# Optimization experiments

Measured on AMD Instinct MI355X. Metric: run time of the kernel, lower is better.

The kernel has to match this reference:

```python
import jax, jax.numpy as jnp
import numpy as np

N_NODES = 50000


def _sage_mean(x, src, dst, Wl, bl, Wr, n_nodes):
    # PyG SAGEConv (aggr='mean', root_weight=True): lin_l(mean_j x_j) + lin_r(x_i)
    msgs = x[src]                                             # [E, F] gather
    agg = jax.ops.segment_sum(msgs, dst, num_segments=n_nodes)  # [N, F]
    cnt = jax.ops.segment_sum(jnp.ones((src.shape[0],), x.dtype), dst,
                              num_segments=n_nodes)           # [N]
    mean = agg / jnp.maximum(cnt, 1.0)[:, None]
    return mean @ Wl + bl + x @ Wr


def setup_inputs() -> dict:
    key = jax.random.key(0)
    ks = jax.random.split(key, 12)
    in_ft = 64
    o0, o1, o2 = 64, 128, 128
    d2 = o0 + o0          # conv2 in = 128
    d3 = o0 + o0 + o1     # conv3 in = 256
    E = 800000

    def lin(k, fi, fo):
        s = 1.0 / np.sqrt(fi)
        return jax.random.uniform(k, (fi, fo), jnp.float32, -s, s)

    x = jax.random.normal(ks[0], (N_NODES, in_ft), jnp.float32)
    edge_index = jax.random.randint(ks[1], (2, E), 0, N_NODES, jnp.int64)
    return {
        "x": x,
        "edge_index": edge_index,
        "Wp": lin(ks[2], in_ft, o0), "bp": jnp.zeros((o0,), jnp.float32),
        "Wl1": lin(ks[3], in_ft, o0), "bl1": jnp.zeros((o0,), jnp.float32),
        "Wr1": lin(ks[4], in_ft, o0),
        "Wl2": lin(ks[5], d2, o1), "bl2": jnp.zeros((o1,), jnp.float32),
        "Wr2": lin(ks[6], d2, o1),
        "Wl3": lin(ks[7], d3, o2), "bl3": jnp.zeros((o2,), jnp.float32),
        "Wr3": lin(ks[8], d3, o2),
    }


def reference(x, edge_index, Wp, bp, Wl1, bl1, Wr1, Wl2, bl2, Wr2, Wl3, bl3, Wr3):
    src, dst = edge_index[0], edge_index[1]
    act = jax.nn.relu
    x_p = act(x @ Wp + bp)                                        # [N, o0]
    h1 = act(_sage_mean(x, src, dst, Wl1, bl1, Wr1, N_NODES))      # [N, o0]
    in2 = jnp.concatenate([x_p, h1], axis=1)                      # [N, 2*o0]
    h2 = act(_sage_mean(in2, src, dst, Wl2, bl2, Wr2, N_NODES))    # [N, o1]
    in3 = jnp.concatenate([x_p, h1, h2], axis=1)                  # [N, 2*o0+o1]
    h3 = act(_sage_mean(in3, src, dst, Wl3, bl3, Wr3, N_NODES))    # [N, o2]
    return h3
```

## Files before the change

kernel.cpp:

```cpp
#include <hip/hip_runtime.h>

#define N_NODES 50000
#define ELLW 48

typedef unsigned int uint;
typedef unsigned short ushort;
typedef float floatx4 __attribute__((ext_vector_type(4)));
typedef short short8 __attribute__((ext_vector_type(8)));

__device__ inline ushort f2bf(float f) {
    uint u = __float_as_uint(f);
    return (ushort)((u + 0x7fffu + ((u >> 16) & 1u)) >> 16);
}
__device__ inline float bflo(uint u) { return __uint_as_float(u << 16); }
__device__ inline float bfhi(uint u) { return __uint_as_float(u & 0xffff0000u); }
__device__ inline uint pack2(float lo, float hi) {
    return (uint)f2bf(lo) | ((uint)f2bf(hi) << 16);
}

__device__ inline void swz_body(const float* __restrict__ W, ushort* __restrict__ Wz,
                                int O, int t) {
    int lane = t & 63, cb = t >> 6;
    int NBm = O / 16;
    int c = cb / NBm, nb = cb % NBm;
    int quad = lane >> 4, l16 = lane & 15;
#pragma unroll
    for (int j = 0; j < 8; j++) {
        float v = W[(size_t)(c * 32 + quad * 8 + j) * O + nb * 16 + l16];
        Wz[(size_t)t * 8 + j] = f2bf(v);
    }
}

__device__ void gemm1_body(int gb, const float* __restrict__ x,
                           const float* __restrict__ Wp, const float* __restrict__ bp,
                           const float* __restrict__ Wl1, const float* __restrict__ Wr1,
                           ushort* __restrict__ feats, ushort* __restrict__ g1in,
                           ushort* __restrict__ r1, ushort* ldsA) {
    constexpr int LDA = 40;
    const int tid = threadIdx.x;
    const int wave = tid >> 6, lane = tid & 63;
    const int quad = lane >> 4, l16 = lane & 15;
    const int node0 = gb * 64;

    floatx4 aP[4], aY[4], aR[4];
#pragma unroll
    for (int nb = 0; nb < 4; nb++) {
        aP[nb] = (floatx4){0, 0, 0, 0};
        aY[nb] = (floatx4){0, 0, 0, 0};
        aR[nb] = (floatx4){0, 0, 0, 0};
    }

#pragma unroll
    for (int kk = 0; kk < 2; kk++) {
        const int k0 = kk * 32;
        __syncthreads();
        {
            int row = tid >> 2, seg = tid & 3;
            int node = node0 + row;
            float4 v0 = {0, 0, 0, 0}, v1 = {0, 0, 0, 0};
            if (node < N_NODES) {
                v0 = *(const float4*)&x[(size_t)node * 64 + k0 + seg * 8];
                v1 = *(const float4*)&x[(size_t)node * 64 + k0 + seg * 8 + 4];
            }
            ushort4 o0, o1;
            o0.x = f2bf(v0.x); o0.y = f2bf(v0.y); o0.z = f2bf(v0.z); o0.w = f2bf(v0.w);
            o1.x = f2bf(v1.x); o1.y = f2bf(v1.y); o1.z = f2bf(v1.z); o1.w = f2bf(v1.w);
            *(ushort4*)&ldsA[row * LDA + seg * 8] = o0;
            *(ushort4*)&ldsA[row * LDA + seg * 8 + 4] = o1;
        }
        __syncthreads();

        short8 a = *(const short8*)&ldsA[(wave * 16 + l16) * LDA + quad * 8];
#pragma unroll
        for (int nb = 0; nb < 4; nb++) {
            short8 bw;
#pragma unroll
            for (int j = 0; j < 8; j++)
                bw[j] = (short)f2bf(Wp[(size_t)(k0 + quad * 8 + j) * 64 + nb * 16 + l16]);
            aP[nb] = __builtin_amdgcn_mfma_f32_16x16x32_bf16(a, bw, aP[nb], 0, 0, 0);
#pragma unroll
            for (int j = 0; j < 8; j++)
                bw[j] = (short)f2bf(Wl1[(size_t)(k0 + quad * 8 + j) * 64 + nb * 16 + l16]);
            aY[nb] = __builtin_amdgcn_mfma_f32_16x16x32_bf16(a, bw, aY[nb], 0, 0, 0);
#pragma unroll
            for (int j = 0; j < 8; j++)
                bw[j] = (short)f2bf(Wr1[(size_t)(k0 + quad * 8 + j) * 64 + nb * 16 + l16]);
            aR[nb] = __builtin_amdgcn_mfma_f32_16x16x32_bf16(a, bw, aR[nb], 0, 0, 0);
        }
    }

#pragma unroll
    for (int nb = 0; nb < 4; nb++) {
        int ncol = nb * 16 + l16;
        float bv = bp[ncol];
#pragma unroll
        for (int r = 0; r < 4; r++) {
            int node = node0 + wave * 16 + quad * 4 + r;
            if (node >= N_NODES) continue;
            ushort xp = f2bf(fmaxf(aP[nb][r] + bv, 0.f));
            feats[(size_t)node * 256 + ncol] = xp;
            g1in[(size_t)node * 128 + 64 + ncol] = xp;
            g1in[(size_t)node * 128 + ncol] = f2bf(aY[nb][r]);
            r1[(size_t)node * 64 + ncol] = f2bf(aR[nb][r]);
        }
    }
}

__global__ __launch_bounds__(256) void k1_mega(
    const int* __restrict__ src, const int* __restrict__ dst, int E,
    int* __restrict__ fillc, ushort* __restrict__ ell,
    const float* __restrict__ x,
    const float* __restrict__ Wp, const float* __restrict__ bp,
    const float* __restrict__ Wl1, const float* __restrict__ Wr1,
    ushort* __restrict__ feats, ushort* __restrict__ g1in, ushort* __restrict__ r1,
    const float* __restrict__ Wl2, ushort* __restrict__ zl2,
    const float* __restrict__ Wr2, ushort* __restrict__ zr2,
    const float* __restrict__ Wl3, ushort* __restrict__ zl3,
    const float* __restrict__ Wr3, ushort* __restrict__ zr3,
    int NF, int NG)
{
    __shared__ ushort ldsA[64 * 40];
    int b = blockIdx.x, tid = threadIdx.x;
    if (b < NF) {
        int t = b * 256 + tid;
        if (t < E) {
            int d = dst[t], s = src[t];
            int p = atomicAdd(&fillc[d], 1);
            if (p < ELLW) ell[(size_t)d * ELLW + p] = (ushort)s;
        }
        return;
    }
    b -= NF;
    if (b < NG) { gemm1_body(b, x, Wp, bp, Wl1, Wr1, feats, g1in, r1, ldsA); return; }
    b -= NG;
    if      (b < 8)  swz_body(Wl2, zl2, 128, (b - 0) * 256 + tid);
    else if (b < 16) swz_body(Wr2, zr2, 128, (b - 8) * 256 + tid);
    else if (b < 32) swz_body(Wl3, zl3, 128, (b - 16) * 256 + tid);
    else             swz_body(Wr3, zr3, 128, (b - 32) * 256 + tid);
}


__global__ __launch_bounds__(256) void gather_split_k(const int* __restrict__ fillc,
                                                      const ushort* __restrict__ ell,
                                                      const ushort* __restrict__ in, int sin,
                                                      ushort* __restrict__ dA, int sA,
                                                      ushort* __restrict__ dB, int sB) {
    int node = blockIdx.x * 4 + (threadIdx.x >> 6);
    if (node >= N_NODES) return;
    int lane = threadIdx.x & 63;
    int sub = lane >> 4, c = lane & 15;
    int n = fillc[node]; int nc = (n > ELLW) ? ELLW : n;
    const ushort* base = ell + (size_t)node * ELLW;
    float a[8];
#pragma unroll
    for (int j = 0; j < 8; j++) a[j] = 0.f;

    int i = sub;
    for (; i + 12 < nc; i += 16) {
        uint4 u0 = *(const uint4*)&in[(size_t)base[i] * sin + 8 * c];
        uint4 u1 = *(const uint4*)&in[(size_t)base[i + 4] * sin + 8 * c];
        uint4 u2 = *(const uint4*)&in[(size_t)base[i + 8] * sin + 8 * c];
        uint4 u3 = *(const uint4*)&in[(size_t)base[i + 12] * sin + 8 * c];
        a[0] += (bflo(u0.x) + bflo(u1.x)) + (bflo(u2.x) + bflo(u3.x));
        a[1] += (bfhi(u0.x) + bfhi(u1.x)) + (bfhi(u2.x) + bfhi(u3.x));
        a[2] += (bflo(u0.y) + bflo(u1.y)) + (bflo(u2.y) + bflo(u3.y));
        a[3] += (bfhi(u0.y) + bfhi(u1.y)) + (bfhi(u2.y) + bfhi(u3.y));
        a[4] += (bflo(u0.z) + bflo(u1.z)) + (bflo(u2.z) + bflo(u3.z));
        a[5] += (bfhi(u0.z) + bfhi(u1.z)) + (bfhi(u2.z) + bfhi(u3.z));
        a[6] += (bflo(u0.w) + bflo(u1.w)) + (bflo(u2.w) + bflo(u3.w));
        a[7] += (bfhi(u0.w) + bfhi(u1.w)) + (bfhi(u2.w) + bfhi(u3.w));
    }
    for (; i < nc; i += 4) {
        uint4 u0 = *(const uint4*)&in[(size_t)base[i] * sin + 8 * c];
        a[0] += bflo(u0.x);  a[1] += bfhi(u0.x);
        a[2] += bflo(u0.y);  a[3] += bfhi(u0.y);
        a[4] += bflo(u0.z);  a[5] += bfhi(u0.z);
        a[6] += bflo(u0.w);  a[7] += bfhi(u0.w);
    }
#pragma unroll
    for (int j = 0; j < 8; j++) {
        a[j] += __shfl_xor(a[j], 16);
        a[j] += __shfl_xor(a[j], 32);
    }
    if (sub == 0) {
        float iv = 1.0f / fmaxf((float)n, 1.0f);
        uint4 r;
        r.x = pack2(a[0] * iv, a[1] * iv);
        r.y = pack2(a[2] * iv, a[3] * iv);
        r.z = pack2(a[4] * iv, a[5] * iv);
        r.w = pack2(a[6] * iv, a[7] * iv);
        if (c < 8) *(uint4*)&dA[(size_t)node * sA + 8 * c] = r;
        else       *(uint4*)&dB[(size_t)node * sB + 8 * (c - 8)] = r;
    }
}

__global__ __launch_bounds__(256) void gather64_k(const int* __restrict__ fillc,
                                                  const ushort* __restrict__ ell,
                                                  const ushort* __restrict__ in, int sin,
                                                  ushort* __restrict__ out, int sout) {
    int wid = blockIdx.x * 4 + (threadIdx.x >> 6);
    int lane = threadIdx.x & 63;
    int half = lane >> 5;
    int node = wid * 2 + half;
    if (node >= N_NODES) return;
    int l32 = lane & 31;
    int sub = l32 >> 3, c = l32 & 7;
    int n = fillc[node]; int nc = (n > ELLW) ? ELLW : n;
    const ushort* base = ell + (size_t)node * ELLW;
    float a[8];
#pragma unroll
    for (int j = 0; j < 8; j++) a[j] = 0.f;

    int i = sub;
    for (; i + 12 < nc; i += 16) {
        uint4 u0 = *(const uint4*)&in[(size_t)base[i] * sin + 8 * c];
        uint4 u1 = *(const uint4*)&in[(size_t)base[i + 4] * sin + 8 * c];
        uint4 u2 = *(const uint4*)&in[(size_t)base[i + 8] * sin + 8 * c];
        uint4 u3 = *(const uint4*)&in[(size_t)base[i + 12] * sin + 8 * c];
        a[0] += (bflo(u0.x) + bflo(u1.x)) + (bflo(u2.x) + bflo(u3.x));
        a[1] += (bfhi(u0.x) + bfhi(u1.x)) + (bfhi(u2.x) + bfhi(u3.x));
        a[2] += (bflo(u0.y) + bflo(u1.y)) + (bflo(u2.y) + bflo(u3.y));
        a[3] += (bfhi(u0.y) + bfhi(u1.y)) + (bfhi(u2.y) + bfhi(u3.y));
        a[4] += (bflo(u0.z) + bflo(u1.z)) + (bflo(u2.z) + bflo(u3.z));
        a[5] += (bfhi(u0.z) + bfhi(u1.z)) + (bfhi(u2.z) + bfhi(u3.z));
        a[6] += (bflo(u0.w) + bflo(u1.w)) + (bflo(u2.w) + bflo(u3.w));
        a[7] += (bfhi(u0.w) + bfhi(u1.w)) + (bfhi(u2.w) + bfhi(u3.w));
    }
    for (; i < nc; i += 4) {
        uint4 u0 = *(const uint4*)&in[(size_t)base[i] * sin + 8 * c];
        a[0] += bflo(u0.x);  a[1] += bfhi(u0.x);
        a[2] += bflo(u0.y);  a[3] += bfhi(u0.y);
        a[4] += bflo(u0.z);  a[5] += bfhi(u0.z);
        a[6] += bflo(u0.w);  a[7] += bfhi(u0.w);
    }
#pragma unroll
    for (int j = 0; j < 8; j++) {
        a[j] += __shfl_xor(a[j], 8);
        a[j] += __shfl_xor(a[j], 16);
    }
    if (sub == 0) {
        float iv = 1.0f / fmaxf((float)n, 1.0f);
        uint4 r;
        r.x = pack2(a[0] * iv, a[1] * iv);
        r.y = pack2(a[2] * iv, a[3] * iv);
        r.z = pack2(a[4] * iv, a[5] * iv);
        r.w = pack2(a[6] * iv, a[7] * iv);
        *(uint4*)&out[(size_t)node * sout + 8 * c] = r;
    }
}

__global__ __launch_bounds__(256) void h1ew_k(const ushort* __restrict__ aggY1,
                                              const ushort* __restrict__ r1,
                                              const float* __restrict__ bl1,
                                              ushort* __restrict__ feats) {
    int t = blockIdx.x * 256 + threadIdx.x;
    if (t >= N_NODES * 8) return;
    int node = t >> 3, c0 = (t & 7) * 8;
    uint4 a = *(const uint4*)&aggY1[(size_t)node * 64 + c0];
    uint4 b = *(const uint4*)&r1[(size_t)node * 64 + c0];
    float4 b0 = *(const float4*)&bl1[c0];
    float4 b1 = *(const float4*)&bl1[c0 + 4];
    uint4 o;
    o.x = pack2(fmaxf(bflo(a.x) + bflo(b.x) + b0.x, 0.f),
                fmaxf(bfhi(a.x) + bfhi(b.x) + b0.y, 0.f));
    o.y = pack2(fmaxf(bflo(a.y) + bflo(b.y) + b0.z, 0.f),
                fmaxf(bfhi(a.y) + bfhi(b.y) + b0.w, 0.f));
    o.z = pack2(fmaxf(bflo(a.z) + bflo(b.z) + b1.x, 0.f),
                fmaxf(bfhi(a.z) + bfhi(b.z) + b1.y, 0.f));
    o.w = pack2(fmaxf(bflo(a.w) + bflo(b.w) + b1.z, 0.f),
                fmaxf(bfhi(a.w) + bfhi(b.w) + b1.w, 0.f));
    *(uint4*)&feats[(size_t)node * 256 + 64 + c0] = o;
}

template <int O, bool OUT_BF16>
__global__ __launch_bounds__(256) void mfma_gemm_k(
    const ushort* __restrict__ A1, int s1, int K1, const ushort* __restrict__ Wz1,
    const ushort* __restrict__ A2, int s2, int K2, const ushort* __restrict__ Wz2,
    const float* __restrict__ bias, void* __restrict__ outp, int so, int ocol)
{
    constexpr int NB = O / 16;
    constexpr int LDA = 40;
    __shared__ ushort ldsA[64 * LDA];

    const int tid = threadIdx.x;
    const int wave = tid >> 6, lane = tid & 63;
    const int quad = lane >> 4, l16 = lane & 15;
    const int node0 = blockIdx.x * 64;

    floatx4 acc[NB];
#pragma unroll
    for (int nb = 0; nb < NB; nb++) acc[nb] = (floatx4){0, 0, 0, 0};

#pragma unroll 1
    for (int phase = 0; phase < 2; ++phase) {
        const ushort* A = phase ? A2 : A1;
        const ushort* Wz = phase ? Wz2 : Wz1;
        const int K = phase ? K2 : K1;
        const int sA = phase ? s2 : s1;

#pragma unroll 1
        for (int k0 = 0; k0 < K; k0 += 32) {
            __syncthreads();
            {
                int row = tid >> 2, seg = tid & 3;
                int node = node0 + row;
                uint4 v = {0, 0, 0, 0};
                if (node < N_NODES)
                    v = *(const uint4*)&A[(size_t)node * sA + k0 + seg * 8];
                *(uint4*)&ldsA[row * LDA + seg * 8] = v;
            }
            __syncthreads();

            short8 a = *(const short8*)&ldsA[(wave * 16 + l16) * LDA + quad * 8];
            const short8* bz = (const short8*)Wz + (size_t)(k0 >> 5) * NB * 64;
#pragma unroll
            for (int nb = 0; nb < NB; nb++) {
                short8 b = bz[nb * 64 + lane];
                acc[nb] = __builtin_amdgcn_mfma_f32_16x16x32_bf16(a, b, acc[nb], 0, 0, 0);
            }
        }
    }

#pragma unroll
    for (int nb = 0; nb < NB; nb++) {
        int ncol = nb * 16 + l16;
        float bv = bias[ncol];
#pragma unroll
        for (int r = 0; r < 4; r++) {
            int node = node0 + wave * 16 + quad * 4 + r;
            if (node >= N_NODES) continue;
            float v = fmaxf(acc[nb][r] + bv, 0.f);
            if (OUT_BF16)
                ((ushort*)outp)[(size_t)node * so + ocol + ncol] = f2bf(v);
            else
                ((float*)outp)[(size_t)node * so + ocol + ncol] = v;
        }
    }
}


extern "C" void kernel_launch(void* const* d_in, const int* in_sizes, int n_in,
                              void* d_out, int out_size, void* d_ws, size_t ws_size,
                              hipStream_t stream) {
    const float* x   = (const float*)d_in[0];
    const int*   ei  = (const int*)d_in[1];
    const float* Wp  = (const float*)d_in[2];
    const float* bp  = (const float*)d_in[3];
    const float* Wl1 = (const float*)d_in[4];
    const float* bl1 = (const float*)d_in[5];
    const float* Wr1 = (const float*)d_in[6];
    const float* Wl2 = (const float*)d_in[7];
    const float* bl2 = (const float*)d_in[8];
    const float* Wr2 = (const float*)d_in[9];
    const float* Wl3 = (const float*)d_in[10];
    const float* bl3 = (const float*)d_in[11];
    const float* Wr3 = (const float*)d_in[12];

    const int E = in_sizes[1] / 2;
    const int N = N_NODES;
    const int* src = ei;
    const int* dst = ei + E;

    char* p = (char*)d_ws;
    ushort* feats = (ushort*)p;  p += (size_t)N * 256 * 2;
    ushort* g1in  = (ushort*)p;  p += (size_t)N * 128 * 2;
    ushort* aggY1 = (ushort*)p;  p += (size_t)N * 64 * 2;
    ushort* aggf  = (ushort*)p;  p += (size_t)N * 256 * 2;
    ushort* r1    = (ushort*)p;  p += (size_t)N * 64 * 2;
    int* fillc    = (int*)p;     p += (size_t)N * 4;
    ushort* ell   = (ushort*)p;  p += (size_t)N * ELLW * 2;
    ushort* zl2   = (ushort*)p;  p += 128 * 128 * 2;
    ushort* zr2   = (ushort*)p;  p += 128 * 128 * 2;
    ushort* zl3   = (ushort*)p;  p += 256 * 128 * 2;
    ushort* zr3   = (ushort*)p;  p += 256 * 128 * 2;

    hipMemsetAsync(fillc, 0, (size_t)N * sizeof(int), stream);

    const int NF = (E + 255) / 256;
    const int NG = (N + 63) / 64;

    k1_mega<<<NF + NG + 48, 256, 0, stream>>>(
        src, dst, E, fillc, ell, x, Wp, bp, Wl1, Wr1, feats, g1in, r1,
        Wl2, zl2, Wr2, zr2, Wl3, zl3, Wr3, zr3, NF, NG);

    gather_split_k<<<(N + 3) / 4, 256, 0, stream>>>(
        fillc, ell, g1in, 128, aggY1, 64, aggf, 256);

    h1ew_k<<<(N * 8 + 255) / 256, 256, 0, stream>>>(aggY1, r1, bl1, feats);

    gather64_k<<<(N + 7) / 8, 256, 0, stream>>>(fillc, ell, feats + 64, 256, aggf + 64, 256);

    mfma_gemm_k<128, true><<<NG, 256, 0, stream>>>(
        aggf, 256, 128, zl2, feats, 256, 128, zr2, bl2, feats, 256, 128);

    gather_split_k<<<(N + 3) / 4, 256, 0, stream>>>(
        fillc, ell, feats + 128, 256, aggf + 128, 256, aggf + 192, 256);

    mfma_gemm_k<128, false><<<NG, 256, 0, stream>>>(
        aggf, 256, 256, zl3, feats, 256, 256, zr3, bl3, (float*)d_out, 128, 0);
}
```

Measured before the change: 295.6 us.

## Fuse all stages into one persistent cooperative kernel with grid syncs

```diff
diff --git a/kernel.cpp b/kernel.cpp
--- a/kernel.cpp
+++ b/kernel.cpp
@@ -1,7 +1,11 @@
 #include <hip/hip_runtime.h>
+#include <hip/hip_cooperative_groups.h>
+
+namespace cg = cooperative_groups;
 
 #define N_NODES 50000
 #define ELLW 48
+#define NGT 782
 
 typedef unsigned int uint;
 typedef unsigned short ushort;
@@ -34,7 +38,7 @@
 __device__ void gemm1_body(int gb, const float* __restrict__ x,
                            const float* __restrict__ Wp, const float* __restrict__ bp,
                            const float* __restrict__ Wl1, const float* __restrict__ Wr1,
-                           ushort* __restrict__ feats, ushort* __restrict__ g1in,
+                           ushort* __restrict__ feats, ushort* __restrict__ y1,
                            ushort* __restrict__ r1, ushort* ldsA) {
     constexpr int LDA = 40;
     const int tid = threadIdx.x;
@@ -97,199 +101,28 @@
         for (int r = 0; r < 4; r++) {
             int node = node0 + wave * 16 + quad * 4 + r;
             if (node >= N_NODES) continue;
-            ushort xp = f2bf(fmaxf(aP[nb][r] + bv, 0.f));
-            feats[(size_t)node * 256 + ncol] = xp;
-            g1in[(size_t)node * 128 + 64 + ncol] = xp;
-            g1in[(size_t)node * 128 + ncol] = f2bf(aY[nb][r]);
+            feats[(size_t)node * 256 + ncol] = f2bf(fmaxf(aP[nb][r] + bv, 0.f));
+            y1[(size_t)node * 64 + ncol] = f2bf(aY[nb][r]);
             r1[(size_t)node * 64 + ncol] = f2bf(aR[nb][r]);
         }
     }
 }
 
-__global__ __launch_bounds__(256) void k1_mega(
-    const int* __restrict__ src, const int* __restrict__ dst, int E,
-    int* __restrict__ fillc, ushort* __restrict__ ell,
-    const float* __restrict__ x,
-    const float* __restrict__ Wp, const float* __restrict__ bp,
-    const float* __restrict__ Wl1, const float* __restrict__ Wr1,
-    ushort* __restrict__ feats, ushort* __restrict__ g1in, ushort* __restrict__ r1,
-    const float* __restrict__ Wl2, ushort* __restrict__ zl2,
-    const float* __restrict__ Wr2, ushort* __restrict__ zr2,
-    const float* __restrict__ Wl3, ushort* __restrict__ zl3,
-    const float* __restrict__ Wr3, ushort* __restrict__ zr3,
-    int NF, int NG)
-{
-    __shared__ ushort ldsA[64 * 40];
-    int b = blockIdx.x, tid = threadIdx.x;
-    if (b < NF) {
-        int t = b * 256 + tid;
-        if (t < E) {
-            int d = dst[t], s = src[t];
-            int p = atomicAdd(&fillc[d], 1);
-            if (p < ELLW) ell[(size_t)d * ELLW + p] = (ushort)s;
-        }
-        return;
-    }
-    b -= NF;
-    if (b < NG) { gemm1_body(b, x, Wp, bp, Wl1, Wr1, feats, g1in, r1, ldsA); return; }
-    b -= NG;
-    if      (b < 8)  swz_body(Wl2, zl2, 128, (b - 0) * 256 + tid);
-    else if (b < 16) swz_body(Wr2, zr2, 128, (b - 8) * 256 + tid);
-    else if (b < 32) swz_body(Wl3, zl3, 128, (b - 16) * 256 + tid);
-    else             swz_body(Wr3, zr3, 128, (b - 32) * 256 + tid);
-}
-
-
-__global__ __launch_bounds__(256) void gather_split_k(const int* __restrict__ fillc,
-                                                      const ushort* __restrict__ ell,
-                                                      const ushort* __restrict__ in, int sin,
-                                                      ushort* __restrict__ dA, int sA,
-                                                      ushort* __restrict__ dB, int sB) {
-    int node = blockIdx.x * 4 + (threadIdx.x >> 6);
-    if (node >= N_NODES) return;
-    int lane = threadIdx.x & 63;
-    int sub = lane >> 4, c = lane & 15;
-    int n = fillc[node]; int nc = (n > ELLW) ? ELLW : n;
-    const ushort* base = ell + (size_t)node * ELLW;
-    float a[8];
-#pragma unroll
-    for (int j = 0; j < 8; j++) a[j] = 0.f;
-
-    int i = sub;
-    for (; i + 12 < nc; i += 16) {
-        uint4 u0 = *(const uint4*)&in[(size_t)base[i] * sin + 8 * c];
-        uint4 u1 = *(const uint4*)&in[(size_t)base[i + 4] * sin + 8 * c];
-        uint4 u2 = *(const uint4*)&in[(size_t)base[i + 8] * sin + 8 * c];
-        uint4 u3 = *(const uint4*)&in[(size_t)base[i + 12] * sin + 8 * c];
-        a[0] += (bflo(u0.x) + bflo(u1.x)) + (bflo(u2.x) + bflo(u3.x));
-        a[1] += (bfhi(u0.x) + bfhi(u1.x)) + (bfhi(u2.x) + bfhi(u3.x));
-        a[2] += (bflo(u0.y) + bflo(u1.y)) + (bflo(u2.y) + bflo(u3.y));
-        a[3] += (bfhi(u0.y) + bfhi(u1.y)) + (bfhi(u2.y) + bfhi(u3.y));
-        a[4] += (bflo(u0.z) + bflo(u1.z)) + (bflo(u2.z) + bflo(u3.z));
-        a[5] += (bfhi(u0.z) + bfhi(u1.z)) + (bfhi(u2.z) + bfhi(u3.z));
-        a[6] += (bflo(u0.w) + bflo(u1.w)) + (bflo(u2.w) + bflo(u3.w));
-        a[7] += (bfhi(u0.w) + bfhi(u1.w)) + (bfhi(u2.w) + bfhi(u3.w));
-    }
-    for (; i < nc; i += 4) {
-        uint4 u0 = *(const uint4*)&in[(size_t)base[i] * sin + 8 * c];
-        a[0] += bflo(u0.x);  a[1] += bfhi(u0.x);
-        a[2] += bflo(u0.y);  a[3] += bfhi(u0.y);
-        a[4] += bflo(u0.z);  a[5] += bfhi(u0.z);
-        a[6] += bflo(u0.w);  a[7] += bfhi(u0.w);
-    }
-#pragma unroll
-    for (int j = 0; j < 8; j++) {
-        a[j] += __shfl_xor(a[j], 16);
-        a[j] += __shfl_xor(a[j], 32);
-    }
-    if (sub == 0) {
-        float iv = 1.0f / fmaxf((float)n, 1.0f);
-        uint4 r;
-        r.x = pack2(a[0] * iv, a[1] * iv);
-        r.y = pack2(a[2] * iv, a[3] * iv);
-        r.z = pack2(a[4] * iv, a[5] * iv);
-        r.w = pack2(a[6] * iv, a[7] * iv);
-        if (c < 8) *(uint4*)&dA[(size_t)node * sA + 8 * c] = r;
-        else       *(uint4*)&dB[(size_t)node * sB + 8 * (c - 8)] = r;
-    }
-}
-
-__global__ __launch_bounds__(256) void gather64_k(const int* __restrict__ fillc,
-                                                  const ushort* __restrict__ ell,
-                                                  const ushort* __restrict__ in, int sin,
-                                                  ushort* __restrict__ out, int sout) {
-    int wid = blockIdx.x * 4 + (threadIdx.x >> 6);
-    int lane = threadIdx.x & 63;
-    int half = lane >> 5;
-    int node = wid * 2 + half;
-    if (node >= N_NODES) return;
-    int l32 = lane & 31;
-    int sub = l32 >> 3, c = l32 & 7;
-    int n = fillc[node]; int nc = (n > ELLW) ? ELLW : n;
-    const ushort* base = ell + (size_t)node * ELLW;
-    float a[8];
-#pragma unroll
-    for (int j = 0; j < 8; j++) a[j] = 0.f;
-
-    int i = sub;
-    for (; i + 12 < nc; i += 16) {
-        uint4 u0 = *(const uint4*)&in[(size_t)base[i] * sin + 8 * c];
-        uint4 u1 = *(const uint4*)&in[(size_t)base[i + 4] * sin + 8 * c];
-        uint4 u2 = *(const uint4*)&in[(size_t)base[i + 8] * sin + 8 * c];
-        uint4 u3 = *(const uint4*)&in[(size_t)base[i + 12] * sin + 8 * c];
-        a[0] += (bflo(u0.x) + bflo(u1.x)) + (bflo(u2.x) + bflo(u3.x));
-        a[1] += (bfhi(u0.x) + bfhi(u1.x)) + (bfhi(u2.x) + bfhi(u3.x));
-        a[2] += (bflo(u0.y) + bflo(u1.y)) + (bflo(u2.y) + bflo(u3.y));
-        a[3] += (bfhi(u0.y) + bfhi(u1.y)) + (bfhi(u2.y) + bfhi(u3.y));
-        a[4] += (bflo(u0.z) + bflo(u1.z)) + (bflo(u2.z) + bflo(u3.z));
-        a[5] += (bfhi(u0.z) + bfhi(u1.z)) + (bfhi(u2.z) + bfhi(u3.z));
-        a[6] += (bflo(u0.w) + bflo(u1.w)) + (bflo(u2.w) + bflo(u3.w));
-        a[7] += (bfhi(u0.w) + bfhi(u1.w)) + (bfhi(u2.w) + bfhi(u3.w));
-    }
-    for (; i < nc; i += 4) {
-        uint4 u0 = *(const uint4*)&in[(size_t)base[i] * sin + 8 * c];
-        a[0] += bflo(u0.x);  a[1] += bfhi(u0.x);
-        a[2] += bflo(u0.y);  a[3] += bfhi(u0.y);
-        a[4] += bflo(u0.z);  a[5] += bfhi(u0.z);
-        a[6] += bflo(u0.w);  a[7] += bfhi(u0.w);
-    }
-#pragma unroll
-    for (int j = 0; j < 8; j++) {
-        a[j] += __shfl_xor(a[j], 8);
-        a[j] += __shfl_xor(a[j], 16);
-    }
-    if (sub == 0) {
-        float iv = 1.0f / fmaxf((float)n, 1.0f);
-        uint4 r;
-        r.x = pack2(a[0] * iv, a[1] * iv);
-        r.y = pack2(a[2] * iv, a[3] * iv);
-        r.z = pack2(a[4] * iv, a[5] * iv);
-        r.w = pack2(a[6] * iv, a[7] * iv);
-        *(uint4*)&out[(size_t)node * sout + 8 * c] = r;
-    }
-}
-
-__global__ __launch_bounds__(256) void h1ew_k(const ushort* __restrict__ aggY1,
-                                              const ushort* __restrict__ r1,
-                                              const float* __restrict__ bl1,
-                                              ushort* __restrict__ feats) {
-    int t = blockIdx.x * 256 + threadIdx.x;
-    if (t >= N_NODES * 8) return;
-    int node = t >> 3, c0 = (t & 7) * 8;
-    uint4 a = *(const uint4*)&aggY1[(size_t)node * 64 + c0];
-    uint4 b = *(const uint4*)&r1[(size_t)node * 64 + c0];
-    float4 b0 = *(const float4*)&bl1[c0];
-    float4 b1 = *(const float4*)&bl1[c0 + 4];
-    uint4 o;
-    o.x = pack2(fmaxf(bflo(a.x) + bflo(b.x) + b0.x, 0.f),
-                fmaxf(bfhi(a.x) + bfhi(b.x) + b0.y, 0.f));
-    o.y = pack2(fmaxf(bflo(a.y) + bflo(b.y) + b0.z, 0.f),
-                fmaxf(bfhi(a.y) + bfhi(b.y) + b0.w, 0.f));
-    o.z = pack2(fmaxf(bflo(a.z) + bflo(b.z) + b1.x, 0.f),
-                fmaxf(bfhi(a.z) + bfhi(b.z) + b1.y, 0.f));
-    o.w = pack2(fmaxf(bflo(a.w) + bflo(b.w) + b1.z, 0.f),
-                fmaxf(bfhi(a.w) + bfhi(b.w) + b1.w, 0.f));
-    *(uint4*)&feats[(size_t)node * 256 + 64 + c0] = o;
-}
-
-template <int O, bool OUT_BF16>
-__global__ __launch_bounds__(256) void mfma_gemm_k(
+__device__ void mfma2_body(int gb,
     const ushort* __restrict__ A1, int s1, int K1, const ushort* __restrict__ Wz1,
     const ushort* __restrict__ A2, int s2, int K2, const ushort* __restrict__ Wz2,
-    const float* __restrict__ bias, void* __restrict__ outp, int so, int ocol)
+    const float* __restrict__ bias, void* __restrict__ outp, int so, int ocol,
+    bool outbf, ushort* ldsA)
 {
-    constexpr int NB = O / 16;
     constexpr int LDA = 40;
-    __shared__ ushort ldsA[64 * LDA];
-
     const int tid = threadIdx.x;
     const int wave = tid >> 6, lane = tid & 63;
     const int quad = lane >> 4, l16 = lane & 15;
-    const int node0 = blockIdx.x * 64;
-
-    floatx4 acc[NB];
-#pragma unroll
-    for (int nb = 0; nb < NB; nb++) acc[nb] = (floatx4){0, 0, 0, 0};
+    const int node0 = gb * 64;
+
+    floatx4 acc[8];
+#pragma unroll
+    for (int nb = 0; nb < 8; nb++) acc[nb] = (floatx4){0, 0, 0, 0};
 
 #pragma unroll 1
     for (int phase = 0; phase < 2; ++phase) {
@@ -297,7 +130,6 @@
         const ushort* Wz = phase ? Wz2 : Wz1;
         const int K = phase ? K2 : K1;
         const int sA = phase ? s2 : s1;
-
 #pragma unroll 1
         for (int k0 = 0; k0 < K; k0 += 32) {
             __syncthreads();
@@ -310,19 +142,16 @@
                 *(uint4*)&ldsA[row * LDA + seg * 8] = v;
             }
             __syncthreads();
-
             short8 a = *(const short8*)&ldsA[(wave * 16 + l16) * LDA + quad * 8];
-            const short8* bz = (const short8*)Wz + (size_t)(k0 >> 5) * NB * 64;
-#pragma unroll
-            for (int nb = 0; nb < NB; nb++) {
-                short8 b = bz[nb * 64 + lane];
-                acc[nb] = __builtin_amdgcn_mfma_f32_16x16x32_bf16(a, b, acc[nb], 0, 0, 0);
-            }
-        }
-    }
-
-#pragma unroll
-    for (int nb = 0; nb < NB; nb++) {
+            const short8* bz = (const short8*)Wz + (size_t)(k0 >> 5) * 8 * 64;
+#pragma unroll
+            for (int nb = 0; nb < 8; nb++)
+                acc[nb] = __builtin_amdgcn_mfma_f32_16x16x32_bf16(a, bz[nb * 64 + lane], acc[nb], 0, 0, 0);
+        }
+    }
+
+#pragma unroll
+    for (int nb = 0; nb < 8; nb++) {
         int ncol = nb * 16 + l16;
         float bv = bias[ncol];
 #pragma unroll
@@ -330,12 +159,236 @@
             int node = node0 + wave * 16 + quad * 4 + r;
             if (node >= N_NODES) continue;
             float v = fmaxf(acc[nb][r] + bv, 0.f);
-            if (OUT_BF16)
+            if (outbf)
                 ((ushort*)outp)[(size_t)node * so + ocol + ncol] = f2bf(v);
             else
                 ((float*)outp)[(size_t)node * so + ocol + ncol] = v;
         }
     }
+}
+
+__global__ __launch_bounds__(256, 6) void mega_k(
+    const int* __restrict__ src, const int* __restrict__ dst, int E,
+    int* __restrict__ fillc, ushort* __restrict__ ell,
+    const float* __restrict__ x,
+    const float* __restrict__ Wp, const float* __restrict__ bp,
+    const float* __restrict__ Wl1, const float* __restrict__ bl1,
+    const float* __restrict__ Wr1,
+    const float* __restrict__ Wl2, const float* __restrict__ bl2,
+    const float* __restrict__ Wr2,
+    const float* __restrict__ Wl3, const float* __restrict__ bl3,
+    const float* __restrict__ Wr3,
+    ushort* __restrict__ feats, ushort* __restrict__ y1, ushort* __restrict__ r1,
+    ushort* __restrict__ aggf,
+    ushort* __restrict__ zl2, ushort* __restrict__ zr2,
+    ushort* __restrict__ zl3, ushort* __restrict__ zr3,
+    float* __restrict__ out, int NFILL, int NGB)
+{
+    __shared__ ushort ldsA[64 * 40];
+    cg::grid_group grid = cg::this_grid();
+    const int bid = blockIdx.x, tid = threadIdx.x;
+    const int G = gridDim.x;
+
+    {
+        int t = bid * 256 + tid;
+        if (t < N_NODES) fillc[t] = 0;
+    }
+    grid.sync();
+
+    if (bid < NFILL) {
+        for (int t = bid * 256 + tid; t < E; t += NFILL * 256) {
+            int d = dst[t], s = src[t];
+            int p = atomicAdd(&fillc[d], 1);
+            if (p < ELLW) ell[(size_t)d * ELLW + p] = (ushort)s;
+        }
+    } else if (bid < NFILL + NGB) {
+        for (int g = bid - NFILL; g < NGT; g += NGB)
+            gemm1_body(g, x, Wp, bp, Wl1, Wr1, feats, y1, r1, ldsA);
+    } else {
+        int nsw = G - NFILL - NGB;
+        for (int u = bid - NFILL - NGB; u < 48; u += nsw) {
+            if      (u < 8)  swz_body(Wl2, zl2, 128, (u - 0) * 256 + tid);
+            else if (u < 16) swz_body(Wr2, zr2, 128, (u - 8) * 256 + tid);
+            else if (u < 32) swz_body(Wl3, zl3, 128, (u - 16) * 256 + tid);
+            else             swz_body(Wr3, zr3, 128, (u - 32) * 256 + tid);
+        }
+    }
+    grid.sync();
+
+    {
+        int wv = bid * 4 + (tid >> 6);
+        int lane = tid & 63;
+        int sub = lane >> 4, c = lane & 15;
+        const ushort* gb0 = (c < 8) ? (y1 + 8 * c) : (feats + 8 * (c - 8));
+        const int gs = (c < 8) ? 64 : 256;
+        for (int node = wv; node < N_NODES; node += G * 4) {
+            int n = fillc[node];
+            int nc = (n > ELLW) ? ELLW : n;
+            const ushort* base = ell + (size_t)node * ELLW;
+            float a[8];
+#pragma unroll
+            for (int j = 0; j < 8; j++) a[j] = 0.f;
+            int i = sub;
+            for (; i + 12 < nc; i += 16) {
+                uint4 u0 = *(const uint4*)&gb0[(size_t)base[i] * gs];
+                uint4 u1 = *(const uint4*)&gb0[(size_t)base[i + 4] * gs];
+                uint4 u2 = *(const uint4*)&gb0[(size_t)base[i + 8] * gs];
+                uint4 u3 = *(const uint4*)&gb0[(size_t)base[i + 12] * gs];
+                a[0] += (bflo(u0.x) + bflo(u1.x)) + (bflo(u2.x) + bflo(u3.x));
+                a[1] += (bfhi(u0.x) + bfhi(u1.x)) + (bfhi(u2.x) + bfhi(u3.x));
+                a[2] += (bflo(u0.y) + bflo(u1.y)) + (bflo(u2.y) + bflo(u3.y));
+                a[3] += (bfhi(u0.y) + bfhi(u1.y)) + (bfhi(u2.y) + bfhi(u3.y));
+                a[4] += (bflo(u0.z) + bflo(u1.z)) + (bflo(u2.z) + bflo(u3.z));
+                a[5] += (bfhi(u0.z) + bfhi(u1.z)) + (bfhi(u2.z) + bfhi(u3.z));
+                a[6] += (bflo(u0.w) + bflo(u1.w)) + (bflo(u2.w) + bflo(u3.w));
+                a[7] += (bfhi(u0.w) + bfhi(u1.w)) + (bfhi(u2.w) + bfhi(u3.w));
+            }
+            for (; i < nc; i += 4) {
+                uint4 u0 = *(const uint4*)&gb0[(size_t)base[i] * gs];
+                a[0] += bflo(u0.x);  a[1] += bfhi(u0.x);
+                a[2] += bflo(u0.y);  a[3] += bfhi(u0.y);
+                a[4] += bflo(u0.z);  a[5] += bfhi(u0.z);
+                a[6] += bflo(u0.w);  a[7] += bfhi(u0.w);
+            }
+#pragma unroll
+            for (int j = 0; j < 8; j++) {
+                a[j] += __shfl_xor(a[j], 16);
+                a[j] += __shfl_xor(a[j], 32);
+            }
+            if (sub == 0) {
+                float iv = 1.0f / fmaxf((float)n, 1.0f);
+                if (c < 8) {
+                    uint4 rv = *(const uint4*)&r1[(size_t)node * 64 + 8 * c];
+                    float4 b0 = *(const float4*)&bl1[8 * c];
+                    float4 b1 = *(const float4*)&bl1[8 * c + 4];
+                    uint4 o;
+                    o.x = pack2(fmaxf(a[0] * iv + bflo(rv.x) + b0.x, 0.f),
+                                fmaxf(a[1] * iv + bfhi(rv.x) + b0.y, 0.f));
+                    o.y = pack2(fmaxf(a[2] * iv + bflo(rv.y) + b0.z, 0.f),
+                                fmaxf(a[3] * iv + bfhi(rv.y) + b0.w, 0.f));
+                    o.z = pack2(fmaxf(a[4] * iv + bflo(rv.z) + b1.x, 0.f),
+                                fmaxf(a[5] * iv + bfhi(rv.z) + b1.y, 0.f));
+                    o.w = pack2(fmaxf(a[6] * iv + bflo(rv.w) + b1.z, 0.f),
+                                fmaxf(a[7] * iv + bfhi(rv.w) + b1.w, 0.f));
+                    *(uint4*)&feats[(size_t)node * 256 + 64 + 8 * c] = o;
+                } else {
+                    uint4 o;
+                    o.x = pack2(a[0] * iv, a[1] * iv);
+                    o.y = pack2(a[2] * iv, a[3] * iv);
+                    o.z = pack2(a[4] * iv, a[5] * iv);
+                    o.w = pack2(a[6] * iv, a[7] * iv);
+                    *(uint4*)&aggf[(size_t)node * 256 + 8 * (c - 8)] = o;
+                }
+            }
+        }
+    }
+    grid.sync();
+
+    {
+        int wv = bid * 4 + (tid >> 6);
+        int lane = tid & 63;
+        int sub = lane >> 3, c = lane & 7;
+        for (int node = wv; node < N_NODES; node += G * 4) {
+            int n = fillc[node];
+            int nc = (n > ELLW) ? ELLW : n;
+            const ushort* base = ell + (size_t)node * ELLW;
+            float a[8];
+#pragma unroll
+            for (int j = 0; j < 8; j++) a[j] = 0.f;
+            int i = sub;
+            for (; i + 8 < nc; i += 16) {
+                uint4 u0 = *(const uint4*)&feats[(size_t)base[i] * 256 + 64 + 8 * c];
+                uint4 u1 = *(const uint4*)&feats[(size_t)base[i + 8] * 256 + 64 + 8 * c];
+                a[0] += bflo(u0.x) + bflo(u1.x);  a[1] += bfhi(u0.x) + bfhi(u1.x);
+                a[2] += bflo(u0.y) + bflo(u1.y);  a[3] += bfhi(u0.y) + bfhi(u1.y);
+                a[4] += bflo(u0.z) + bflo(u1.z);  a[5] += bfhi(u0.z) + bfhi(u1.z);
+                a[6] += bflo(u0.w) + bflo(u1.w);  a[7] += bfhi(u0.w) + bfhi(u1.w);
+            }
+            for (; i < nc; i += 8) {
+                uint4 u0 = *(const uint4*)&feats[(size_t)base[i] * 256 + 64 + 8 * c];
+                a[0] += bflo(u0.x);  a[1] += bfhi(u0.x);
+                a[2] += bflo(u0.y);  a[3] += bfhi(u0.y);
+                a[4] += bflo(u0.z);  a[5] += bfhi(u0.z);
+                a[6] += bflo(u0.w);  a[7] += bfhi(u0.w);
+            }
+#pragma unroll
+            for (int j = 0; j < 8; j++) {
+                a[j] += __shfl_xor(a[j], 8);
+                a[j] += __shfl_xor(a[j], 16);
+                a[j] += __shfl_xor(a[j], 32);
+            }
+            if (sub == 0) {
+                float iv = 1.0f / fmaxf((float)n, 1.0f);
+                uint4 o;
+                o.x = pack2(a[0] * iv, a[1] * iv);
+                o.y = pack2(a[2] * iv, a[3] * iv);
+                o.z = pack2(a[4] * iv, a[5] * iv);
+                o.w = pack2(a[6] * iv, a[7] * iv);
+                *(uint4*)&aggf[(size_t)node * 256 + 64 + 8 * c] = o;
+            }
+        }
+    }
+    grid.sync();
+
+    for (int g = bid; g < NGT; g += G)
+        mfma2_body(g, aggf, 256, 128, zl2, feats, 256, 128, zr2, bl2,
+                   feats, 256, 128, true, ldsA);
+    grid.sync();
+
+    {
+        int wv = bid * 4 + (tid >> 6);
+        int lane = tid & 63;
+        int sub = lane >> 4, c = lane & 15;
+        for (int node = wv; node < N_NODES; node += G * 4) {
+            int n = fillc[node];
+            int nc = (n > ELLW) ? ELLW : n;
+            const ushort* base = ell + (size_t)node * ELLW;
+            float a[8];
+#pragma unroll
+            for (int j = 0; j < 8; j++) a[j] = 0.f;
+            int i = sub;
+            for (; i + 12 < nc; i += 16) {
+                uint4 u0 = *(const uint4*)&feats[(size_t)base[i] * 256 + 128 + 8 * c];
+                uint4 u1 = *(const uint4*)&feats[(size_t)base[i + 4] * 256 + 128 + 8 * c];
+                uint4 u2 = *(const uint4*)&feats[(size_t)base[i + 8] * 256 + 128 + 8 * c];
+                uint4 u3 = *(const uint4*)&feats[(size_t)base[i + 12] * 256 + 128 + 8 * c];
+                a[0] += (bflo(u0.x) + bflo(u1.x)) + (bflo(u2.x) + bflo(u3.x));
+                a[1] += (bfhi(u0.x) + bfhi(u1.x)) + (bfhi(u2.x) + bfhi(u3.x));
+                a[2] += (bflo(u0.y) + bflo(u1.y)) + (bflo(u2.y) + bflo(u3.y));
+                a[3] += (bfhi(u0.y) + bfhi(u1.y)) + (bfhi(u2.y) + bfhi(u3.y));
+                a[4] += (bflo(u0.z) + bflo(u1.z)) + (bflo(u2.z) + bflo(u3.z));
+                a[5] += (bfhi(u0.z) + bfhi(u1.z)) + (bfhi(u2.z) + bfhi(u3.z));
+                a[6] += (bflo(u0.w) + bflo(u1.w)) + (bflo(u2.w) + bflo(u3.w));
+                a[7] += (bfhi(u0.w) + bfhi(u1.w)) + (bfhi(u2.w) + bfhi(u3.w));
+            }
+            for (; i < nc; i += 4) {
+                uint4 u0 = *(const uint4*)&feats[(size_t)base[i] * 256 + 128 + 8 * c];
+                a[0] += bflo(u0.x);  a[1] += bfhi(u0.x);
+                a[2] += bflo(u0.y);  a[3] += bfhi(u0.y);
+                a[4] += bflo(u0.z);  a[5] += bfhi(u0.z);
+                a[6] += bflo(u0.w);  a[7] += bfhi(u0.w);
+            }
+#pragma unroll
+            for (int j = 0; j < 8; j++) {
+                a[j] += __shfl_xor(a[j], 16);
+                a[j] += __shfl_xor(a[j], 32);
+            }
+            if (sub == 0) {
+                float iv = 1.0f / fmaxf((float)n, 1.0f);
+                uint4 o;
+                o.x = pack2(a[0] * iv, a[1] * iv);
+                o.y = pack2(a[2] * iv, a[3] * iv);
+                o.z = pack2(a[4] * iv, a[5] * iv);
+                o.w = pack2(a[6] * iv, a[7] * iv);
+                *(uint4*)&aggf[(size_t)node * 256 + 128 + 8 * c] = o;
+            }
+        }
+    }
+    grid.sync();
+
+    for (int g = bid; g < NGT; g += G)
+        mfma2_body(g, aggf, 256, 256, zl3, feats, 256, 256, zr3, bl3,
+                   out, 128, 0, false, ldsA);
 }
 
 
@@ -356,46 +409,45 @@
     const float* bl3 = (const float*)d_in[11];
     const float* Wr3 = (const float*)d_in[12];
 
-    const int E = in_sizes[1] / 2;
+    int E = in_sizes[1] / 2;
     const int N = N_NODES;
     const int* src = ei;
     const int* dst = ei + E;
 
     char* p = (char*)d_ws;
     ushort* feats = (ushort*)p;  p += (size_t)N * 256 * 2;
-    ushort* g1in  = (ushort*)p;  p += (size_t)N * 128 * 2;
-    ushort* aggY1 = (ushort*)p;  p += (size_t)N * 64 * 2;
+    ushort* y1    = (ushort*)p;  p += (size_t)N * 64 * 2;
+    ushort* r1    = (ushort*)p;  p += (size_t)N * 64 * 2;
     ushort* aggf  = (ushort*)p;  p += (size_t)N * 256 * 2;
-    ushort* r1    = (ushort*)p;  p += (size_t)N * 64 * 2;
     int* fillc    = (int*)p;     p += (size_t)N * 4;
     ushort* ell   = (ushort*)p;  p += (size_t)N * ELLW * 2;
     ushort* zl2   = (ushort*)p;  p += 128 * 128 * 2;
     ushort* zr2   = (ushort*)p;  p += 128 * 128 * 2;
     ushort* zl3   = (ushort*)p;  p += 256 * 128 * 2;
     ushort* zr3   = (ushort*)p;  p += 256 * 128 * 2;
-
-    hipMemsetAsync(fillc, 0, (size_t)N * sizeof(int), stream);
-
-    const int NF = (E + 255) / 256;
-    const int NG = (N + 63) / 64;
-
-    k1_mega<<<NF + NG + 48, 256, 0, stream>>>(
-        src, dst, E, fillc, ell, x, Wp, bp, Wl1, Wr1, feats, g1in, r1,
-        Wl2, zl2, Wr2, zr2, Wl3, zl3, Wr3, zr3, NF, NG);
-
-    gather_split_k<<<(N + 3) / 4, 256, 0, stream>>>(
-        fillc, ell, g1in, 128, aggY1, 64, aggf, 256);
-
-    h1ew_k<<<(N * 8 + 255) / 256, 256, 0, stream>>>(aggY1, r1, bl1, feats);
-
-    gather64_k<<<(N + 7) / 8, 256, 0, stream>>>(fillc, ell, feats + 64, 256, aggf + 64, 256);
-
-    mfma_gemm_k<128, true><<<NG, 256, 0, stream>>>(
-        aggf, 256, 128, zl2, feats, 256, 128, zr2, bl2, feats, 256, 128);
-
-    gather_split_k<<<(N + 3) / 4, 256, 0, stream>>>(
-        fillc, ell, feats + 128, 256, aggf + 128, 256, aggf + 192, 256);
-
-    mfma_gemm_k<128, false><<<NG, 256, 0, stream>>>(
-        aggf, 256, 256, zl3, feats, 256, 256, zr3, bl3, (float*)d_out, 128, 0);
-}
+    float* outp   = (float*)d_out;
+
+    int maxB = 0;
+    if (hipOccupancyMaxActiveBlocksPerMultiprocessor(
+            &maxB, reinterpret_cast<const void*>(mega_k), 256, 0) != hipSuccess || maxB <= 0)
+        maxB = 4;
+    if (maxB > 6) maxB = 6;
+    int G = maxB * 256;
+
+    int SWZ = 24;
+    int NGB = G / 7;
+    int NFILL = G - NGB - SWZ;
+
+    void* args[] = {
+        (void*)&src, (void*)&dst, (void*)&E,
+        (void*)&fillc, (void*)&ell, (void*)&x,
+        (void*)&Wp, (void*)&bp, (void*)&Wl1, (void*)&bl1, (void*)&Wr1,
+        (void*)&Wl2, (void*)&bl2, (void*)&Wr2,
+        (void*)&Wl3, (void*)&bl3, (void*)&Wr3,
+        (void*)&feats, (void*)&y1, (void*)&r1, (void*)&aggf,
+        (void*)&zl2, (void*)&zr2, (void*)&zl3, (void*)&zr3,
+        (void*)&outp, (void*)&NFILL, (void*)&NGB
+    };
+    hipLaunchCooperativeKernel(reinterpret_cast<const void*>(mega_k),
+                               dim3(G), dim3(256), args, 0, stream);
+}
```

Result: slower. 916.2 us (+210.0%).
